# Kernel optimization log

Hardware: AMD Instinct MI355X
Metric: run time of the kernel (lower is better)

## Reference

```python
import jax, jax.numpy as jnp
import numpy as np

LN_EPS = 1e-5


def setup_inputs() -> dict:
    key = jax.random.key(0)
    ks = jax.random.split(key, 4)
    S, B, C, V, TS = 512, 64, 1024, 10, 128
    sc = 1.0 / np.sqrt(C)
    return {
        "values": jax.random.normal(ks[0], (S, B, C), dtype=jnp.float32),
        "Wd": jax.random.normal(ks[1], (3, C), dtype=jnp.float32) * sc,
        "bd": jnp.zeros((3,), jnp.float32),
        "Wr": jax.random.normal(ks[2], (2, C), dtype=jnp.float32) * sc,
        "br": jnp.zeros((2,), jnp.float32),
        "ln_g": jnp.ones((C,), jnp.float32),
        "ln_b": jnp.zeros((C,), jnp.float32),
        "Wo": jax.random.normal(ks[3], (V, C), dtype=jnp.float32) * sc,
        "bo": jnp.zeros((V,), jnp.float32),
        "tsize": TS,
    }


def _nam_turing(values, Wd, bd, Wr, br, ln_g, ln_b, Wo, bo, tsize):
    S, B, C = values.shape
    # training-mode addressing: soft softmax over 3 move directions
    directions = jax.nn.softmax(values @ Wd.T + bd, axis=-1)  # [S,B,3]
    rwprobs = jax.nn.sigmoid(values @ Wr.T + br)              # [S,B,2]

    tape0 = jnp.zeros((tsize, B, C), values.dtype)
    pos0 = jnp.zeros((tsize, B), values.dtype).at[0, :].set(1.0)

    def step(carry, xs):
        tape, pos = carry
        v, d, rw = xs  # [B,C], [B,3], [B,2]
        oldval = jnp.einsum("lnc,ln->nc", tape, pos)
        # outer-product write gated by write prob rw[:,1]
        tape = tape + pos[:, :, None] * ((v - oldval) * rw[:, 1:2])[None]
        pos = (jnp.roll(pos, -1, axis=0) * d[None, :, 0]
               + pos * d[None, :, 1]
               + jnp.roll(pos, 1, axis=0) * d[None, :, 2])
        return (tape, pos), None

    (tape, _), _ = jax.lax.scan(step, (tape0, pos0), (values, directions, rwprobs))

    # decoder: LayerNorm -> (dropout as identity) -> Linear
    mu = jnp.mean(tape, axis=-1, keepdims=True)
    var = jnp.mean(jnp.square(tape - mu), axis=-1, keepdims=True)
    h = (tape - mu) * jax.lax.rsqrt(var + LN_EPS) * ln_g + ln_b
    return h @ Wo.T + bo  # [tsize, B, V]


def reference(values, Wd, bd, Wr, br, ln_g, ln_b, Wo, bo, tsize):
    return _nam_turing(values, Wd, bd, Wr, br, ln_g, ln_b, Wo, bo, tsize)
```

## Files before the change

### kernel.cpp

```cpp
#include <hip/hip_runtime.h>
#include <math.h>

#define S_ 512
#define B_ 64
#define C_ 1024
#define T_ 128
#define V_ 10
#define LN_EPS 1e-5f

#define DPP_ADD(x, ctrl)                                                     \
    ((x) + __int_as_float(__builtin_amdgcn_update_dpp(                       \
               0, __float_as_int(x), (ctrl), 0xf, 0xf, true)))

__global__ __launch_bounds__(256) void k_dirs(const float* __restrict__ values,
                                              const float* __restrict__ Wd,
                                              const float* __restrict__ bd,
                                              const float* __restrict__ Wr,
                                              const float* __restrict__ br,
                                              float* __restrict__ dtr) {
    int wid  = (blockIdx.x << 2) + (threadIdx.x >> 6);
    int lane = threadIdx.x & 63;
    const float4* v4  = (const float4*)(values + (size_t)wid * C_);
    const float4* wd4 = (const float4*)Wd;
    const float4* wr4 = (const float4*)Wr;
    float a0 = 0.f, a1 = 0.f, a2 = 0.f, a3 = 0.f;
#pragma unroll
    for (int k = 0; k < 4; k++) {
        int i = (k << 6) + lane;
        float4 v  = v4[i];
        float4 w0 = wd4[i];
        float4 w1 = wd4[256 + i];
        float4 w2 = wd4[512 + i];
        float4 w3 = wr4[256 + i];
        a0 = fmaf(v.x, w0.x, fmaf(v.y, w0.y, fmaf(v.z, w0.z, fmaf(v.w, w0.w, a0))));
        a1 = fmaf(v.x, w1.x, fmaf(v.y, w1.y, fmaf(v.z, w1.z, fmaf(v.w, w1.w, a1))));
        a2 = fmaf(v.x, w2.x, fmaf(v.y, w2.y, fmaf(v.z, w2.z, fmaf(v.w, w2.w, a2))));
        a3 = fmaf(v.x, w3.x, fmaf(v.y, w3.y, fmaf(v.z, w3.z, fmaf(v.w, w3.w, a3))));
    }
#pragma unroll
    for (int m = 1; m < 64; m <<= 1) {
        a0 += __shfl_xor(a0, m, 64);
        a1 += __shfl_xor(a1, m, 64);
        a2 += __shfl_xor(a2, m, 64);
        a3 += __shfl_xor(a3, m, 64);
    }
    if (lane == 0) {
        float l0 = a0 + bd[0], l1 = a1 + bd[1], l2 = a2 + bd[2];
        float mx = fmaxf(fmaxf(l0, l1), l2);
        float e0 = __expf(l0 - mx), e1 = __expf(l1 - mx), e2 = __expf(l2 - mx);
        float inv = 1.f / (e0 + e1 + e2);
        float r = 1.f / (1.f + __expf(-(a3 + br[1])));
        ((float4*)dtr)[wid] = make_float4(e0 * inv, e1 * inv, e2 * inv, r);
    }
}

__global__ __launch_bounds__(64) void k_pos(const float* __restrict__ dtr,
                                            float* __restrict__ pos_all) {
    int b = blockIdx.x;
    int lane = threadIdx.x;
    const float4* dtr4 = (const float4*)dtr;
    float4 dreg[8];
#pragma unroll
    for (int k = 0; k < 8; k++)
        dreg[k] = dtr4[(((size_t)(k << 6) + lane) << 6) + b];
    float p0 = (lane == 0) ? 1.f : 0.f;
    float p1 = 0.f;
    float* outp = pos_all + ((size_t)b << 7) + lane;
    int up = (lane + 1) & 63, dw = (lane + 63) & 63;
#pragma unroll
    for (int k = 0; k < 8; k++) {
#pragma unroll 4
        for (int tt = 0; tt < 64; tt++) {
            int t = (k << 6) + tt;
            float d0 = __shfl(dreg[k].x, tt, 64);
            float d1 = __shfl(dreg[k].y, tt, 64);
            float d2 = __shfl(dreg[k].z, tt, 64);
            outp[(size_t)t * (B_ * T_)]      = p0;
            outp[(size_t)t * (B_ * T_) + 64] = p1;
            float s0n = __shfl(p0, up, 64), s1n = __shfl(p1, up, 64);
            float s0p = __shfl(p0, dw, 64), s1p = __shfl(p1, dw, 64);
            float up0 = (lane == 63) ? s1n : s0n;
            float dn0 = (lane == 0)  ? s1p : s0p;
            float up1 = (lane == 63) ? s0n : s1n;
            float dn1 = (lane == 0)  ? s0p : s1p;
            p0 = fmaf(up0, d0, fmaf(p0, d1, dn0 * d2));
            p1 = fmaf(up1, d0, fmaf(p1, d1, dn1 * d2));
        }
    }
}

__global__ __launch_bounds__(256, 2) void k_scan(const float* __restrict__ values,
                                                 const float* __restrict__ dtr,
                                                 const float* __restrict__ pos_all,
                                                 float* __restrict__ tape_out) {
    const int b    = blockIdx.x >> 3;
    const int cblk = blockIdx.x & 7;
    const int tid  = threadIdx.x;
    const int lane = tid & 63;
    const int wv   = tid >> 6;
    const int g    = lane & 7;
    const int cl   = lane >> 3;
    const int c0   = (cblk << 7) + (wv << 5) + (cl << 2);

    __shared__ float4 pos_s[2][8][32];
    __shared__ float4 v_s[2][8][32];
    __shared__ float  rw_s[2][8];

    float tape[16][4];
#pragma unroll
    for (int k = 0; k < 16; k++)
#pragma unroll
        for (int c = 0; c < 4; c++) tape[k][c] = 0.f;

    const int tl   = tid >> 5;
    const int pi   = tid & 31;
    const int pdst = ((pi & 3) << 3) + (pi >> 2);
    const float4* pos4 = (const float4*)pos_all;
    const float4* val4 = (const float4*)values;
    const size_t  vsrc = (size_t)b * (C_ / 4) + (cblk << 5) + pi;

    {
        pos_s[0][tl][pdst] = pos4[((size_t)tl * B_ + b) * (T_ / 4) + pi];
        v_s[0][tl][pi]     = val4[(size_t)tl * (B_ * C_ / 4) + vsrc];
        if (tid < 8) rw_s[0][tid] = dtr[(((size_t)tid * B_ + b) << 2) + 3];
    }
    __syncthreads();

    int cur = 0;
    for (int ch = 0; ch < S_ / 8; ch++) {
        const int t0n = (ch + 1 < S_ / 8) ? ((ch + 1) << 3) : 0;
        float4 pfp = pos4[((size_t)(t0n + tl) * B_ + b) * (T_ / 4) + pi];
        float4 pfv = val4[(size_t)(t0n + tl) * (B_ * C_ / 4) + vsrc];
        float  pfr = (tid < 8) ? dtr[(((size_t)(t0n + tid) * B_ + b) << 2) + 3] : 0.f;

#pragma unroll
        for (int ts = 0; ts < 8; ts++) {
            float4 pj0 = pos_s[cur][ts][g];
            float4 pj1 = pos_s[cur][ts][8 + g];
            float4 pj2 = pos_s[cur][ts][16 + g];
            float4 pj3 = pos_s[cur][ts][24 + g];
            float4 vv  = v_s[cur][ts][(wv << 3) + cl];
            float  rw  = rw_s[cur][ts];
            float pk[16];
            pk[0]  = pj0.x; pk[1]  = pj0.y; pk[2]  = pj0.z; pk[3]  = pj0.w;
            pk[4]  = pj1.x; pk[5]  = pj1.y; pk[6]  = pj1.z; pk[7]  = pj1.w;
            pk[8]  = pj2.x; pk[9]  = pj2.y; pk[10] = pj2.z; pk[11] = pj2.w;
            pk[12] = pj3.x; pk[13] = pj3.y; pk[14] = pj3.z; pk[15] = pj3.w;

            float ov[4] = {0.f, 0.f, 0.f, 0.f};
#pragma unroll
            for (int k = 0; k < 16; k++) {
                ov[0] = fmaf(tape[k][0], pk[k], ov[0]);
                ov[1] = fmaf(tape[k][1], pk[k], ov[1]);
                ov[2] = fmaf(tape[k][2], pk[k], ov[2]);
                ov[3] = fmaf(tape[k][3], pk[k], ov[3]);
            }
#pragma unroll
            for (int c = 0; c < 4; c++) {
                ov[c] = DPP_ADD(ov[c], 0xB1);
                ov[c] = DPP_ADD(ov[c], 0x4E);
                ov[c] = DPP_ADD(ov[c], 0x141);
            }
            float de[4];
            de[0] = (vv.x - ov[0]) * rw;
            de[1] = (vv.y - ov[1]) * rw;
            de[2] = (vv.z - ov[2]) * rw;
            de[3] = (vv.w - ov[3]) * rw;
#pragma unroll
            for (int k = 0; k < 16; k++) {
                tape[k][0] = fmaf(pk[k], de[0], tape[k][0]);
                tape[k][1] = fmaf(pk[k], de[1], tape[k][1]);
                tape[k][2] = fmaf(pk[k], de[2], tape[k][2]);
                tape[k][3] = fmaf(pk[k], de[3], tape[k][3]);
            }
        }
        int nxt = cur ^ 1;
        pos_s[nxt][tl][pdst] = pfp;
        v_s[nxt][tl][pi]     = pfv;
        if (tid < 8) rw_s[nxt][tid] = pfr;
        __syncthreads();
        cur = nxt;
    }

#pragma unroll
    for (int k = 0; k < 16; k++) {
        int l = (g << 4) + k;
        *(float4*)(tape_out + ((size_t)l * B_ + b) * C_ + c0) =
            make_float4(tape[k][0], tape[k][1], tape[k][2], tape[k][3]);
    }
}

__global__ __launch_bounds__(256) void k_out(const float* __restrict__ tape,
                                             const float* __restrict__ ln_g,
                                             const float* __restrict__ ln_b,
                                             const float* __restrict__ Wo,
                                             const float* __restrict__ bo,
                                             float* __restrict__ out) {
    int wid  = (blockIdx.x << 2) + (threadIdx.x >> 6);
    int lane = threadIdx.x & 63;
    const float* tr = tape + (size_t)wid * C_;
    float x[16];
    float s = 0.f, s2 = 0.f;
#pragma unroll
    for (int k = 0; k < 16; k++) {
        x[k] = tr[(k << 6) + lane];
        s += x[k];
        s2 = fmaf(x[k], x[k], s2);
    }
#pragma unroll
    for (int m = 1; m < 64; m <<= 1) {
        s  += __shfl_xor(s,  m, 64);
        s2 += __shfl_xor(s2, m, 64);
    }
    float mu = s * (1.f / C_);
    float var = s2 * (1.f / C_) - mu * mu;
    float rstd = rsqrtf(var + LN_EPS);
    float acc[V_];
#pragma unroll
    for (int v = 0; v < V_; v++) acc[v] = 0.f;
#pragma unroll
    for (int k = 0; k < 16; k++) {
        int cc = (k << 6) + lane;
        float h = fmaf((x[k] - mu) * rstd, ln_g[cc], ln_b[cc]);
#pragma unroll
        for (int v = 0; v < V_; v++) acc[v] = fmaf(h, Wo[v * C_ + cc], acc[v]);
    }
#pragma unroll
    for (int v = 0; v < V_; v++) {
#pragma unroll
        for (int m = 1; m < 64; m <<= 1) acc[v] += __shfl_xor(acc[v], m, 64);
    }
    if (lane == 0) {
#pragma unroll
        for (int v = 0; v < V_; v++) out[(size_t)wid * V_ + v] = acc[v] + bo[v];
    }
}

extern "C" void kernel_launch(void* const* d_in, const int* in_sizes, int n_in,
                              void* d_out, int out_size, void* d_ws, size_t ws_size,
                              hipStream_t stream) {
    const float* values = (const float*)d_in[0];
    const float* Wd     = (const float*)d_in[1];
    const float* bd     = (const float*)d_in[2];
    const float* Wr     = (const float*)d_in[3];
    const float* br     = (const float*)d_in[4];
    const float* ln_g   = (const float*)d_in[5];
    const float* ln_b   = (const float*)d_in[6];
    const float* Wo     = (const float*)d_in[7];
    const float* bo     = (const float*)d_in[8];
    float* out = (float*)d_out;

    float* dtr     = (float*)d_ws;
    float* pos_all = dtr + (size_t)S_ * B_ * 4;
    float* tape    = pos_all + (size_t)S_ * B_ * T_;

    k_dirs<<<dim3((S_ * B_) / 4), dim3(256), 0, stream>>>(values, Wd, bd, Wr, br, dtr);
    k_pos <<<dim3(B_),            dim3(64),  0, stream>>>(dtr, pos_all);
    k_scan<<<dim3(B_ * 8),        dim3(256), 0, stream>>>(values, dtr, pos_all, tape);
    k_out <<<dim3((T_ * B_) / 4), dim3(256), 0, stream>>>(tape, ln_g, ln_b, Wo, bo, out);
}
```

Before: 488.8 us.

## Batch two scan steps per tape pass via Gram correction; vectorize decoder loads

The scan kernel now processes two time steps per pass over the register-resident tape. It computes both read-outs against the pre-step tape and corrects the second step's delta with the dot product of the two position vectors, then applies both rank-1 updates in one loop. This roughly halves the tape traversals and the loop-carried dependency chain per step, at the cost of an extra reduction and more live registers. The decoder kernel also switches to float4 loads for the tape, LayerNorm parameters and Wo.

```diff
diff --git a/kernel.cpp b/kernel.cpp
--- a/kernel.cpp
+++ b/kernel.cpp
@@ -134,44 +134,73 @@
         float  pfr = (tid < 8) ? dtr[(((size_t)(t0n + tid) * B_ + b) << 2) + 3] : 0.f;
 
 #pragma unroll
-        for (int ts = 0; ts < 8; ts++) {
-            float4 pj0 = pos_s[cur][ts][g];
-            float4 pj1 = pos_s[cur][ts][8 + g];
-            float4 pj2 = pos_s[cur][ts][16 + g];
-            float4 pj3 = pos_s[cur][ts][24 + g];
-            float4 vv  = v_s[cur][ts][(wv << 3) + cl];
-            float  rw  = rw_s[cur][ts];
-            float pk[16];
-            pk[0]  = pj0.x; pk[1]  = pj0.y; pk[2]  = pj0.z; pk[3]  = pj0.w;
-            pk[4]  = pj1.x; pk[5]  = pj1.y; pk[6]  = pj1.z; pk[7]  = pj1.w;
-            pk[8]  = pj2.x; pk[9]  = pj2.y; pk[10] = pj2.z; pk[11] = pj2.w;
-            pk[12] = pj3.x; pk[13] = pj3.y; pk[14] = pj3.z; pk[15] = pj3.w;
-
-            float ov[4] = {0.f, 0.f, 0.f, 0.f};
+        for (int tp = 0; tp < 4; tp++) {
+            const int ts0 = tp << 1, ts1 = ts0 + 1;
+            float4 qa0 = pos_s[cur][ts0][g];
+            float4 qa1 = pos_s[cur][ts0][8 + g];
+            float4 qa2 = pos_s[cur][ts0][16 + g];
+            float4 qa3 = pos_s[cur][ts0][24 + g];
+            float4 qb0 = pos_s[cur][ts1][g];
+            float4 qb1 = pos_s[cur][ts1][8 + g];
+            float4 qb2 = pos_s[cur][ts1][16 + g];
+            float4 qb3 = pos_s[cur][ts1][24 + g];
+            float4 v1  = v_s[cur][ts0][(wv << 3) + cl];
+            float4 v2  = v_s[cur][ts1][(wv << 3) + cl];
+            float  rw1 = rw_s[cur][ts0];
+            float  rw2 = rw_s[cur][ts1];
+            float pk1[16], pk2[16];
+            pk1[0]  = qa0.x; pk1[1]  = qa0.y; pk1[2]  = qa0.z; pk1[3]  = qa0.w;
+            pk1[4]  = qa1.x; pk1[5]  = qa1.y; pk1[6]  = qa1.z; pk1[7]  = qa1.w;
+            pk1[8]  = qa2.x; pk1[9]  = qa2.y; pk1[10] = qa2.z; pk1[11] = qa2.w;
+            pk1[12] = qa3.x; pk1[13] = qa3.y; pk1[14] = qa3.z; pk1[15] = qa3.w;
+            pk2[0]  = qb0.x; pk2[1]  = qb0.y; pk2[2]  = qb0.z; pk2[3]  = qb0.w;
+            pk2[4]  = qb1.x; pk2[5]  = qb1.y; pk2[6]  = qb1.z; pk2[7]  = qb1.w;
+            pk2[8]  = qb2.x; pk2[9]  = qb2.y; pk2[10] = qb2.z; pk2[11] = qb2.w;
+            pk2[12] = qb3.x; pk2[13] = qb3.y; pk2[14] = qb3.z; pk2[15] = qb3.w;
+
+            float a1[4] = {0.f, 0.f, 0.f, 0.f};
+            float a2[4] = {0.f, 0.f, 0.f, 0.f};
+            float gg = 0.f;
 #pragma unroll
             for (int k = 0; k < 16; k++) {
-                ov[0] = fmaf(tape[k][0], pk[k], ov[0]);
-                ov[1] = fmaf(tape[k][1], pk[k], ov[1]);
-                ov[2] = fmaf(tape[k][2], pk[k], ov[2]);
-                ov[3] = fmaf(tape[k][3], pk[k], ov[3]);
+                a1[0] = fmaf(tape[k][0], pk1[k], a1[0]);
+                a1[1] = fmaf(tape[k][1], pk1[k], a1[1]);
+                a1[2] = fmaf(tape[k][2], pk1[k], a1[2]);
+                a1[3] = fmaf(tape[k][3], pk1[k], a1[3]);
+                a2[0] = fmaf(tape[k][0], pk2[k], a2[0]);
+                a2[1] = fmaf(tape[k][1], pk2[k], a2[1]);
+                a2[2] = fmaf(tape[k][2], pk2[k], a2[2]);
+                a2[3] = fmaf(tape[k][3], pk2[k], a2[3]);
+                gg    = fmaf(pk1[k], pk2[k], gg);
             }
 #pragma unroll
             for (int c = 0; c < 4; c++) {
-                ov[c] = DPP_ADD(ov[c], 0xB1);
-                ov[c] = DPP_ADD(ov[c], 0x4E);
-                ov[c] = DPP_ADD(ov[c], 0x141);
+                a1[c] = DPP_ADD(a1[c], 0xB1);
+                a1[c] = DPP_ADD(a1[c], 0x4E);
+                a1[c] = DPP_ADD(a1[c], 0x141);
+                a2[c] = DPP_ADD(a2[c], 0xB1);
+                a2[c] = DPP_ADD(a2[c], 0x4E);
+                a2[c] = DPP_ADD(a2[c], 0x141);
             }
-            float de[4];
-            de[0] = (vv.x - ov[0]) * rw;
-            de[1] = (vv.y - ov[1]) * rw;
-            de[2] = (vv.z - ov[2]) * rw;
-            de[3] = (vv.w - ov[3]) * rw;
+            gg = DPP_ADD(gg, 0xB1);
+            gg = DPP_ADD(gg, 0x4E);
+            gg = DPP_ADD(gg, 0x141);
+
+            float d1[4], d2[4];
+            d1[0] = (v1.x - a1[0]) * rw1;
+            d1[1] = (v1.y - a1[1]) * rw1;
+            d1[2] = (v1.z - a1[2]) * rw1;
+            d1[3] = (v1.w - a1[3]) * rw1;
+            d2[0] = fmaf(-gg, d1[0], v2.x - a2[0]) * rw2;
+            d2[1] = fmaf(-gg, d1[1], v2.y - a2[1]) * rw2;
+            d2[2] = fmaf(-gg, d1[2], v2.z - a2[2]) * rw2;
+            d2[3] = fmaf(-gg, d1[3], v2.w - a2[3]) * rw2;
 #pragma unroll
             for (int k = 0; k < 16; k++) {
-                tape[k][0] = fmaf(pk[k], de[0], tape[k][0]);
-                tape[k][1] = fmaf(pk[k], de[1], tape[k][1]);
-                tape[k][2] = fmaf(pk[k], de[2], tape[k][2]);
-                tape[k][3] = fmaf(pk[k], de[3], tape[k][3]);
+                tape[k][0] = fmaf(pk1[k], d1[0], fmaf(pk2[k], d2[0], tape[k][0]));
+                tape[k][1] = fmaf(pk1[k], d1[1], fmaf(pk2[k], d2[1], tape[k][1]));
+                tape[k][2] = fmaf(pk1[k], d1[2], fmaf(pk2[k], d2[2], tape[k][2]));
+                tape[k][3] = fmaf(pk1[k], d1[3], fmaf(pk2[k], d2[3], tape[k][3]));
             }
         }
         int nxt = cur ^ 1;
@@ -198,14 +227,17 @@
                                              float* __restrict__ out) {
     int wid  = (blockIdx.x << 2) + (threadIdx.x >> 6);
     int lane = threadIdx.x & 63;
-    const float* tr = tape + (size_t)wid * C_;
-    float x[16];
+    const float4* tr4 = (const float4*)(tape + (size_t)wid * C_);
+    float4 x[4];
     float s = 0.f, s2 = 0.f;
 #pragma unroll
-    for (int k = 0; k < 16; k++) {
-        x[k] = tr[(k << 6) + lane];
-        s += x[k];
-        s2 = fmaf(x[k], x[k], s2);
+    for (int j = 0; j < 4; j++) {
+        x[j] = tr4[(j << 6) + lane];
+        s += (x[j].x + x[j].y) + (x[j].z + x[j].w);
+        s2 = fmaf(x[j].x, x[j].x, s2);
+        s2 = fmaf(x[j].y, x[j].y, s2);
+        s2 = fmaf(x[j].z, x[j].z, s2);
+        s2 = fmaf(x[j].w, x[j].w, s2);
     }
 #pragma unroll
     for (int m = 1; m < 64; m <<= 1) {
@@ -218,12 +250,26 @@
     float acc[V_];
 #pragma unroll
     for (int v = 0; v < V_; v++) acc[v] = 0.f;
-#pragma unroll
-    for (int k = 0; k < 16; k++) {
-        int cc = (k << 6) + lane;
-        float h = fmaf((x[k] - mu) * rstd, ln_g[cc], ln_b[cc]);
-#pragma unroll
-        for (int v = 0; v < V_; v++) acc[v] = fmaf(h, Wo[v * C_ + cc], acc[v]);
+    const float4* g4 = (const float4*)ln_g;
+    const float4* b4 = (const float4*)ln_b;
+    const float4* w4 = (const float4*)Wo;
+#pragma unroll
+    for (int j = 0; j < 4; j++) {
+        int ci = (j << 6) + lane;
+        float4 gg = g4[ci], bb = b4[ci];
+        float4 h;
+        h.x = fmaf((x[j].x - mu) * rstd, gg.x, bb.x);
+        h.y = fmaf((x[j].y - mu) * rstd, gg.y, bb.y);
+        h.z = fmaf((x[j].z - mu) * rstd, gg.z, bb.z);
+        h.w = fmaf((x[j].w - mu) * rstd, gg.w, bb.w);
+#pragma unroll
+        for (int v = 0; v < V_; v++) {
+            float4 w = w4[v * (C_ / 4) + ci];
+            acc[v] = fmaf(h.x, w.x, acc[v]);
+            acc[v] = fmaf(h.y, w.y, acc[v]);
+            acc[v] = fmaf(h.z, w.z, acc[v]);
+            acc[v] = fmaf(h.w, w.w, acc[v]);
+        }
     }
 #pragma unroll
     for (int v = 0; v < V_; v++) {
```

After: 502.6 us. 2.8% more time.
